# Performance work log

Hardware: AMD Instinct MI355X
Metric: run time of the kernel (lower is better)

## Reference

```python
import jax, jax.numpy as jnp
import numpy as np

# 8 corner offsets of the trilinear cell: (8, 3)
_OFFS = jnp.array([[i, j, k] for i in (0, 1) for j in (0, 1) for k in (0, 1)], dtype=jnp.int32)


def _gridding(cloud, R):
    """Trilinear scatter of points into an RxRxR occupancy-weight grid.

    cloud: (b, n, 3) with coords in [-0.5, 0.5] (already divided by scale).
    Returns (b, R, R, R) grid where each point adds trilinear weights to its
    8 neighboring cells (the GRNet gridding_distance forward kernel).
    """
    b, n, _ = cloud.shape
    v = (cloud + 0.5) * R                      # continuous voxel coords in [0, R)
    lower = jnp.floor(v)
    frac = v - lower                           # (b, n, 3) in [0, 1)
    lower = lower.astype(jnp.int32)
    nb = lower[:, :, None, :] + _OFFS[None, None]              # (b, n, 8, 3)
    # per-axis trilinear weight: (1 - frac) for the low corner, frac for the high
    w_d = jnp.where(_OFFS[None, None] == 0,
                    1.0 - frac[:, :, None, :], frac[:, :, None, :])  # (b, n, 8, 3)
    w = jnp.prod(w_d, axis=-1)                                  # (b, n, 8)
    valid = jnp.all((nb >= 0) & (nb < R), axis=-1)              # (b, n, 8)
    w = jnp.where(valid, w, 0.0)
    nbc = jnp.clip(nb, 0, R - 1)
    flat = (nbc[..., 0] * R + nbc[..., 1]) * R + nbc[..., 2]    # (b, n, 8)
    batch_off = jnp.arange(b, dtype=jnp.int32)[:, None, None] * (R * R * R)
    idx = (flat + batch_off).reshape(-1)
    grid = jnp.zeros((b * R * R * R,), cloud.dtype).at[idx].add(w.reshape(-1))
    return grid.reshape(b, R, R, R)


def setup_inputs() -> dict:
    key = jax.random.key(0)
    k1, k2 = jax.random.split(key)
    R = 128
    B, N1, N2 = 16, 65536, 65536
    # coords in [-(R-2)/2, (R-2)/2] so that after /scale they are inside (-0.5, 0.5)
    pred = (jax.random.uniform(k1, (B, N1, 3), jnp.float32) - 0.5) * (R - 2)
    gt = (jax.random.uniform(k2, (B, N2, 3), jnp.float32) - 0.5) * (R - 2)
    return {"pred_cloud": pred, "gt_cloud": gt, "scale": R}


def reference(pred_cloud, gt_cloud, scale):
    pred = pred_cloud / scale
    gt = gt_cloud / scale
    return _gridding(pred, scale), _gridding(gt, scale)
```

## Files before the change

### kernel.cpp

```cpp
#include <hip/hip_runtime.h>
#include <stdint.h>


constexpr int R    = 128;
constexpr int R3c  = R * R * R;
constexpr int BPG  = 256;
constexpr int NBLK = 512;
constexpr int BLKT = 512;
constexpr int PPT  = 8;
constexpr int MAXB = 128;
constexpr int MAXSEG = 64;

constexpr size_t WS_HIST = 0;
constexpr size_t WS_PFX  = 1u << 20;
constexpr size_t WS_REC  = 2u << 20;

typedef float f4v __attribute__((ext_vector_type(4)));

__device__ __forceinline__ uint32_t quant1(float p) {
    const float S = 16384.0f;
    const uint32_t QMAX = (126u << 14) | 16383u;
    float v = p + 64.0f;
    return min(__float2uint_rn(fmaxf(v, 0.0f) * S), QMAX);
}

__device__ __forceinline__ uint2 pack_rec(uint32_t xq, uint32_t yq, uint32_t zq) {
    return make_uint2(xq | (yq << 21), (yq >> 11) | (zq << 10));
}
__device__ __forceinline__ void unpack_rec(uint2 r, uint32_t& xq, uint32_t& yq, uint32_t& zq) {
    xq = r.x & 0x1FFFFFu;
    yq = (r.x >> 21) | ((r.y & 0x3FFu) << 11);
    zq = (r.y >> 10) & 0x1FFFFFu;
}

__device__ __forceinline__ void region_range(uint32_t xq, uint32_t yq, uint32_t zq,
                                             int& rx0, int& rx1, int& ry0, int& ry1,
                                             int& rz0, int& rz1)
{
    int ix = xq >> 14, iy = yq >> 14, iz = zq >> 14;
    rx0 = ix >> 4; rx1 = (ix + 1) >> 4;
    ry0 = iy >> 4; ry1 = (iy + 1) >> 4;
    rz0 = iz >> 5; rz1 = (iz + 1) >> 5;
}

__global__ __launch_bounds__(BLKT) void sort_local(
    const float* __restrict__ pred, const float* __restrict__ gt,
    int total1, int capb,
    uint32_t* __restrict__ hist, uint32_t* __restrict__ pfxg,
    uint2* __restrict__ records)
{
    __shared__ uint32_t h[BPG];
    __shared__ uint32_t px[BPG];
    if (threadIdx.x < BPG) h[threadIdx.x] = 0;
    __syncthreads();

    const int ppb = PPT * BLKT;
    int s = blockIdx.x * ppb;
    bool isgt = (s >= total1);
    const float4* src4 = (const float4*)(isgt ? gt + (size_t)(s - total1) * 3
                                              : pred + (size_t)s * 3);
    uint2 lrec[PPT / 4][4];
    #pragma unroll
    for (int it = 0; it < PPT / 4; ++it) {
        int g = threadIdx.x + it * BLKT;
        float4 a  = src4[g * 3 + 0];
        float4 b4 = src4[g * 3 + 1];
        float4 c4 = src4[g * 3 + 2];
        float xs[4] = {a.x, a.w, b4.z, c4.y};
        float ys[4] = {a.y, b4.x, b4.w, c4.z};
        float zs[4] = {a.z, b4.y, c4.x, c4.w};
        #pragma unroll
        for (int q = 0; q < 4; ++q) {
            uint32_t xq = quant1(xs[q]), yq = quant1(ys[q]), zq = quant1(zs[q]);
            lrec[it][q] = pack_rec(xq, yq, zq);
            int rx0, rx1, ry0, ry1, rz0, rz1;
            region_range(xq, yq, zq, rx0, rx1, ry0, ry1, rz0, rz1);
            for (int aa = rx0; aa <= rx1; ++aa)
                for (int bb = ry0; bb <= ry1; ++bb)
                    for (int cc = rz0; cc <= rz1; ++cc)
                        atomicAdd(&h[(aa << 5) + (bb << 2) + cc], 1u);
        }
    }
    __syncthreads();

    if (threadIdx.x < BPG) px[threadIdx.x] = h[threadIdx.x];
    __syncthreads();
    #pragma unroll
    for (int off = 1; off < BPG; off <<= 1) {
        uint32_t v = 0;
        if (threadIdx.x < BPG && threadIdx.x >= (uint32_t)off)
            v = px[threadIdx.x - off];
        __syncthreads();
        if (threadIdx.x < BPG) px[threadIdx.x] += v;
        __syncthreads();
    }
    if (threadIdx.x < BPG) {
        uint32_t excl = px[threadIdx.x] - h[threadIdx.x];
        hist[(size_t)blockIdx.x * BPG + threadIdx.x] = h[threadIdx.x];
        pfxg[(size_t)blockIdx.x * BPG + threadIdx.x] = excl;
        px[threadIdx.x] = excl;
    }
    __syncthreads();

    uint2* rbase = records + (size_t)blockIdx.x * capb;
    #pragma unroll
    for (int it = 0; it < PPT / 4; ++it) {
        #pragma unroll
        for (int q = 0; q < 4; ++q) {
            uint2 rec = lrec[it][q];
            uint32_t xq, yq, zq;
            unpack_rec(rec, xq, yq, zq);
            int rx0, rx1, ry0, ry1, rz0, rz1;
            region_range(xq, yq, zq, rx0, rx1, ry0, ry1, rz0, rz1);
            for (int aa = rx0; aa <= rx1; ++aa)
                for (int bb = ry0; bb <= ry1; ++bb)
                    for (int cc = rz0; cc <= rz1; ++cc) {
                        uint32_t slot = atomicAdd(&px[(aa << 5) + (bb << 2) + cc], 1u);
                        rbase[slot] = rec;
                    }
        }
    }
}

__global__ __launch_bounds__(256) void accum_seg(
    const uint32_t* __restrict__ hist, const uint32_t* __restrict__ pfxg,
    const uint2* __restrict__ records, float* __restrict__ out,
    int B, int nb1, int bpg1, int bpg2, int capb)
{
    __shared__ float tile[16 * 16 * 32];
    __shared__ uint32_t sOff[MAXSEG + 1];
    __shared__ uint32_t sStart[MAXSEG];
    int bin = blockIdx.x;
    int cb = bin >> 8;
    int l  = bin & 255;
    int rx = l >> 5, ry = (l >> 2) & 7, rz = l & 3;

    int first = (cb < B) ? cb * bpg1 : nb1 + (cb - B) * bpg2;
    int cnt   = (cb < B) ? bpg1 : bpg2;

    float4* t4 = (float4*)tile;
    for (int t = threadIdx.x; t < 2048; t += 256)
        t4[t] = make_float4(0.f, 0.f, 0.f, 0.f);
    if (threadIdx.x < (uint32_t)cnt) {
        sStart[threadIdx.x] = pfxg[(size_t)(first + threadIdx.x) * BPG + l];
        sOff[threadIdx.x]   = hist[(size_t)(first + threadIdx.x) * BPG + l];
    }
    __syncthreads();
    if (threadIdx.x == 0) {
        uint32_t run = 0;
        for (int k = 0; k < cnt; ++k) { uint32_t c = sOff[k]; sOff[k] = run; run += c; }
        sOff[cnt] = run;
    }
    __syncthreads();

    uint32_t total = sOff[cnt];
    const float FQ = 6.103515625e-05f;
    for (uint32_t r = threadIdx.x; r < total; r += 256) {
        int lo = 0, hi = cnt - 1;
        while (lo < hi) {
            int mid = (lo + hi + 1) >> 1;
            if (sOff[mid] <= r) lo = mid; else hi = mid - 1;
        }
        uint2 rc = records[(size_t)(first + lo) * capb + sStart[lo] + (r - sOff[lo])];
        uint32_t xq, yq, zq;
        unpack_rec(rc, xq, yq, zq);
        int ix = xq >> 14, iy = yq >> 14, iz = zq >> 14;
        float fx = (float)(xq & 16383u) * FQ;
        float fy = (float)(yq & 16383u) * FQ;
        float fz = (float)(zq & 16383u) * FQ;
        float wx[2] = {1.0f - fx, fx};
        float wy[2] = {1.0f - fy, fy};
        float wz[2] = {1.0f - fz, fz};
        #pragma unroll
        for (int dx = 0; dx < 2; ++dx) {
            int cx = ix + dx;
            if ((cx >> 4) != rx) continue;
            #pragma unroll
            for (int dy = 0; dy < 2; ++dy) {
                int cy = iy + dy;
                if ((cy >> 4) != ry) continue;
                float wxy = wx[dx] * wy[dy];
                #pragma unroll
                for (int dz = 0; dz < 2; ++dz) {
                    int cz = iz + dz;
                    if ((cz >> 5) != rz) continue;
                    atomicAdd(&tile[(((cx & 15) << 4) + (cy & 15)) * 32 + (cz & 31)],
                              wxy * wz[dz]);
                }
            }
        }
    }
    __syncthreads();

    float* gout = out + (size_t)cb * R3c;
    for (int w = threadIdx.x; w < 2048; w += 256) {
        int lin = w * 4;
        int lx = lin >> 9, rem = lin & 511, ly = rem >> 5, lz = rem & 31;
        int X = rx * 16 + lx, Y = ry * 16 + ly, Z = rz * 32 + lz;
        f4v v = ((const f4v*)tile)[w];
        __builtin_nontemporal_store(v, (f4v*)&gout[((size_t)X * R + Y) * R + Z]);
    }
}

__device__ __forceinline__ void point_math_f(float px, float py, float pz,
                                             int& ix, int& iy, int& iz,
                                             float& fx, float& fy, float& fz)
{
    const float inv = 1.0f / 128.0f;
    float vx = (px * inv + 0.5f) * 128.0f;
    float vy = (py * inv + 0.5f) * 128.0f;
    float vz = (pz * inv + 0.5f) * 128.0f;
    float lx = floorf(vx), ly = floorf(vy), lz = floorf(vz);
    fx = vx - lx; fy = vy - ly; fz = vz - lz;
    ix = min(max((int)lx, 0), R - 2);
    iy = min(max((int)ly, 0), R - 2);
    iz = min(max((int)lz, 0), R - 2);
}

__global__ __launch_bounds__(256) void gridding_scatter(
    const float* __restrict__ cloud, float* __restrict__ grid,
    int total_pts, int n_per_batch)
{
    int idx = blockIdx.x * blockDim.x + threadIdx.x;
    if (idx >= total_pts) return;
    int b = idx / n_per_batch;
    const float* p = cloud + (size_t)idx * 3;
    int ix, iy, iz; float fx, fy, fz;
    point_math_f(p[0], p[1], p[2], ix, iy, iz, fx, fy, fz);
    float wx[2] = {1.0f - fx, fx};
    float wy[2] = {1.0f - fy, fy};
    float wz[2] = {1.0f - fz, fz};
    float* gb = grid + (size_t)b * R3c;
    #pragma unroll
    for (int dx = 0; dx < 2; ++dx)
        #pragma unroll
        for (int dy = 0; dy < 2; ++dy) {
            float wxy = wx[dx] * wy[dy];
            #pragma unroll
            for (int dz = 0; dz < 2; ++dz)
                atomicAdd(gb + ((size_t)(ix + dx) * R + (iy + dy)) * R + (iz + dz),
                          wxy * wz[dz]);
        }
}

extern "C" void kernel_launch(void* const* d_in, const int* in_sizes, int n_in,
                              void* d_out, int out_size, void* d_ws, size_t ws_size,
                              hipStream_t stream) {
    const float* pred = (const float*)d_in[0];
    const float* gt   = (const float*)d_in[1];
    float* out = (float*)d_out;

    int total1 = in_sizes[0] / 3;
    int total2 = in_sizes[1] / 3;
    int B  = out_size / (2 * R3c);
    int n1 = (B > 0) ? total1 / B : 0;
    int n2 = (B > 0) ? total2 / B : 0;
    int NBINS = 2 * B * BPG;
    int P  = total1 + total2;
    int ppb = PPT * BLKT;

    int capb = 8 * ppb;
    size_t ws_need = WS_REC + (size_t)NBLK * capb * 8;

    bool fastok = (B > 0) && (B <= MAXB) && (n1 > 0) && (n2 > 0) &&
                  (total1 == B * n1) && (total2 == B * n2) &&
                  (P == NBLK * ppb) &&
                  (n1 % ppb == 0) && (n2 % ppb == 0) &&
                  (n1 / ppb <= MAXSEG) && (n2 / ppb <= MAXSEG) &&
                  (ws_size >= ws_need);
    if (!fastok) {
        hipMemsetAsync(d_out, 0, (size_t)out_size * sizeof(float), stream);
        gridding_scatter<<<(total1 + 255) / 256, 256, 0, stream>>>(pred, out, total1, n1);
        gridding_scatter<<<(total2 + 255) / 256, 256, 0, stream>>>(
            gt, out + (size_t)B * R3c, total2, n2);
        return;
    }

    uint32_t* hist = (uint32_t*)((char*)d_ws + WS_HIST);
    uint32_t* pfxg = (uint32_t*)((char*)d_ws + WS_PFX);
    uint2*    recs = (uint2*)((char*)d_ws + WS_REC);

    int nb1  = total1 / ppb;
    int bpg1 = n1 / ppb;
    int bpg2 = n2 / ppb;

    sort_local<<<NBLK, BLKT, 0, stream>>>(pred, gt, total1, capb, hist, pfxg, recs);
    accum_seg<<<NBINS, 256, 0, stream>>>(hist, pfxg, recs, out,
                                         B, nb1, bpg1, bpg2, capb);
}
```

Before: 364.7 us.

## Stage sorted records in LDS for coalesced writes, halve points per block

The local sort kernel now handles 4 points per thread across twice as many blocks. Bin-sorted records are scattered into an LDS staging buffer first and then copied to global memory contiguously, with a fallback to direct scatter when the block's record count exceeds the buffer capacity. The accumulation kernel uses 512-thread blocks instead of 256. The aim is to replace uncoalesced global scatter writes with coalesced ones and to raise parallelism, at the cost of more LDS per block and more, smaller segments per bin in the accumulation step.

```diff
diff --git a/kernel.cpp b/kernel.cpp
--- a/kernel.cpp
+++ b/kernel.cpp
@@ -5,9 +5,11 @@
 constexpr int R    = 128;
 constexpr int R3c  = R * R * R;
 constexpr int BPG  = 256;
-constexpr int NBLK = 512;
+constexpr int NBLK = 1024;
 constexpr int BLKT = 512;
-constexpr int PPT  = 8;
+constexpr int PPT  = 4;
+constexpr int STCAP = 4096;
+constexpr int ABLK = 512;
 constexpr int MAXB = 128;
 constexpr int MAXSEG = 64;
 
@@ -51,6 +53,8 @@
 {
     __shared__ uint32_t h[BPG];
     __shared__ uint32_t px[BPG];
+    __shared__ uint2 stg[STCAP];
+    __shared__ uint32_t sT;
     if (threadIdx.x < BPG) h[threadIdx.x] = 0;
     __syncthreads();
 
@@ -59,27 +63,24 @@
     bool isgt = (s >= total1);
     const float4* src4 = (const float4*)(isgt ? gt + (size_t)(s - total1) * 3
                                               : pred + (size_t)s * 3);
-    uint2 lrec[PPT / 4][4];
+    int g = threadIdx.x;
+    float4 a  = src4[g * 3 + 0];
+    float4 b4 = src4[g * 3 + 1];
+    float4 c4 = src4[g * 3 + 2];
+    float xs[4] = {a.x, a.w, b4.z, c4.y};
+    float ys[4] = {a.y, b4.x, b4.w, c4.z};
+    float zs[4] = {a.z, b4.y, c4.x, c4.w};
+    uint2 lrec[4];
     #pragma unroll
-    for (int it = 0; it < PPT / 4; ++it) {
-        int g = threadIdx.x + it * BLKT;
-        float4 a  = src4[g * 3 + 0];
-        float4 b4 = src4[g * 3 + 1];
-        float4 c4 = src4[g * 3 + 2];
-        float xs[4] = {a.x, a.w, b4.z, c4.y};
-        float ys[4] = {a.y, b4.x, b4.w, c4.z};
-        float zs[4] = {a.z, b4.y, c4.x, c4.w};
-        #pragma unroll
-        for (int q = 0; q < 4; ++q) {
-            uint32_t xq = quant1(xs[q]), yq = quant1(ys[q]), zq = quant1(zs[q]);
-            lrec[it][q] = pack_rec(xq, yq, zq);
-            int rx0, rx1, ry0, ry1, rz0, rz1;
-            region_range(xq, yq, zq, rx0, rx1, ry0, ry1, rz0, rz1);
-            for (int aa = rx0; aa <= rx1; ++aa)
-                for (int bb = ry0; bb <= ry1; ++bb)
-                    for (int cc = rz0; cc <= rz1; ++cc)
-                        atomicAdd(&h[(aa << 5) + (bb << 2) + cc], 1u);
-        }
+    for (int q = 0; q < 4; ++q) {
+        uint32_t xq = quant1(xs[q]), yq = quant1(ys[q]), zq = quant1(zs[q]);
+        lrec[q] = pack_rec(xq, yq, zq);
+        int rx0, rx1, ry0, ry1, rz0, rz1;
+        region_range(xq, yq, zq, rx0, rx1, ry0, ry1, rz0, rz1);
+        for (int aa = rx0; aa <= rx1; ++aa)
+            for (int bb = ry0; bb <= ry1; ++bb)
+                for (int cc = rz0; cc <= rz1; ++cc)
+                    atomicAdd(&h[(aa << 5) + (bb << 2) + cc], 1u);
     }
     __syncthreads();
 
@@ -94,6 +95,7 @@
         if (threadIdx.x < BPG) px[threadIdx.x] += v;
         __syncthreads();
     }
+    if (threadIdx.x == BPG - 1) sT = px[BPG - 1];
     if (threadIdx.x < BPG) {
         uint32_t excl = px[threadIdx.x] - h[threadIdx.x];
         hist[(size_t)blockIdx.x * BPG + threadIdx.x] = h[threadIdx.x];
@@ -103,11 +105,29 @@
     __syncthreads();
 
     uint2* rbase = records + (size_t)blockIdx.x * capb;
-    #pragma unroll
-    for (int it = 0; it < PPT / 4; ++it) {
+    uint32_t T = sT;
+    if (T <= (uint32_t)STCAP) {
         #pragma unroll
         for (int q = 0; q < 4; ++q) {
-            uint2 rec = lrec[it][q];
+            uint2 rec = lrec[q];
+            uint32_t xq, yq, zq;
+            unpack_rec(rec, xq, yq, zq);
+            int rx0, rx1, ry0, ry1, rz0, rz1;
+            region_range(xq, yq, zq, rx0, rx1, ry0, ry1, rz0, rz1);
+            for (int aa = rx0; aa <= rx1; ++aa)
+                for (int bb = ry0; bb <= ry1; ++bb)
+                    for (int cc = rz0; cc <= rz1; ++cc) {
+                        uint32_t slot = atomicAdd(&px[(aa << 5) + (bb << 2) + cc], 1u);
+                        stg[slot] = rec;
+                    }
+        }
+        __syncthreads();
+        for (uint32_t i = threadIdx.x; i < T; i += BLKT)
+            rbase[i] = stg[i];
+    } else {
+        #pragma unroll
+        for (int q = 0; q < 4; ++q) {
+            uint2 rec = lrec[q];
             uint32_t xq, yq, zq;
             unpack_rec(rec, xq, yq, zq);
             int rx0, rx1, ry0, ry1, rz0, rz1;
@@ -122,7 +142,7 @@
     }
 }
 
-__global__ __launch_bounds__(256) void accum_seg(
+__global__ __launch_bounds__(ABLK) void accum_seg(
     const uint32_t* __restrict__ hist, const uint32_t* __restrict__ pfxg,
     const uint2* __restrict__ records, float* __restrict__ out,
     int B, int nb1, int bpg1, int bpg2, int capb)
@@ -139,7 +159,7 @@
     int cnt   = (cb < B) ? bpg1 : bpg2;
 
     float4* t4 = (float4*)tile;
-    for (int t = threadIdx.x; t < 2048; t += 256)
+    for (int t = threadIdx.x; t < 2048; t += ABLK)
         t4[t] = make_float4(0.f, 0.f, 0.f, 0.f);
     if (threadIdx.x < (uint32_t)cnt) {
         sStart[threadIdx.x] = pfxg[(size_t)(first + threadIdx.x) * BPG + l];
@@ -155,7 +175,7 @@
 
     uint32_t total = sOff[cnt];
     const float FQ = 6.103515625e-05f;
-    for (uint32_t r = threadIdx.x; r < total; r += 256) {
+    for (uint32_t r = threadIdx.x; r < total; r += ABLK) {
         int lo = 0, hi = cnt - 1;
         while (lo < hi) {
             int mid = (lo + hi + 1) >> 1;
@@ -193,7 +213,7 @@
     __syncthreads();
 
     float* gout = out + (size_t)cb * R3c;
-    for (int w = threadIdx.x; w < 2048; w += 256) {
+    for (int w = threadIdx.x; w < 2048; w += ABLK) {
         int lin = w * 4;
         int lx = lin >> 9, rem = lin & 511, ly = rem >> 5, lz = rem & 31;
         int X = rx * 16 + lx, Y = ry * 16 + ly, Z = rz * 32 + lz;
@@ -255,7 +275,6 @@
     int B  = out_size / (2 * R3c);
     int n1 = (B > 0) ? total1 / B : 0;
     int n2 = (B > 0) ? total2 / B : 0;
-    int NBINS = 2 * B * BPG;
     int P  = total1 + total2;
     int ppb = PPT * BLKT;
 
@@ -283,8 +302,9 @@
     int nb1  = total1 / ppb;
     int bpg1 = n1 / ppb;
     int bpg2 = n2 / ppb;
+    int NBINS = 2 * B * BPG;
 
     sort_local<<<NBLK, BLKT, 0, stream>>>(pred, gt, total1, capb, hist, pfxg, recs);
-    accum_seg<<<NBINS, 256, 0, stream>>>(hist, pfxg, recs, out,
-                                         B, nb1, bpg1, bpg2, capb);
-}
+    accum_seg<<<NBINS, ABLK, 0, stream>>>(hist, pfxg, recs, out,
+                                          B, nb1, bpg1, bpg2, capb);
+}
```

After: 356.9 us. -2.1%, faster.
